# Kernel tuning notes

Hardware: AMD Instinct MI355X
Metric: run time of the kernel (lower is better)

Reference implementation:

```python
import jax, jax.numpy as jnp
import numpy as np

R = 3          # routing iterations (init arg r)
EPS = 1e-7     # init arg epsilon


def squash(s, axis=-1):
    # squash(s) = ||s||^2 / (1 + ||s||^2) * s / (||s|| + EPS)
    n = jnp.linalg.norm(s, axis=axis, keepdims=True)
    n2 = jnp.square(n)
    return (n2 / (1.0 + n2)) * (s / (n + EPS))


def setup_inputs() -> dict:
    key = jax.random.key(0)
    k1, k2 = jax.random.split(key)
    B, S, P, J, I = 32, 32, 2048, 32, 16
    inputs = jax.random.normal(k1, (B, P, I), dtype=jnp.float32)
    # tf.random_normal_initializer default stddev = 0.05
    W = jax.random.normal(k2, (S, P, J, I), dtype=jnp.float32) * 0.05
    return {"inputs": inputs, "W": W}


def reference(inputs, W):
    # u_hat[b,s,p,j] = sum_i W[s,p,j,i] * inputs[b,p,i]
    u_hat = jnp.einsum('spji,bpi->bspj', W, inputs)  # [B,S,P,J]
    B, S, P, J = u_hat.shape
    b = jnp.zeros((B, S, 1, P), dtype=u_hat.dtype)
    v = None
    for _ in range(R):
        c = jax.nn.softmax(b, axis=-1)                     # over primary caps
        s = jnp.einsum('bsxp,bspj->bsxj', c, u_hat)        # [B,S,1,J]
        v = squash(s)                                      # [B,S,1,J]
        agreement = jnp.einsum('bsxj,bspj->bsxp', v, u_hat)  # [B,S,1,P]
        b = b + agreement
    return v.reshape(B, S, J)
```

## Files before the change

kernel.cpp:

```cpp
#include <hip/hip_runtime.h>
#include <stdint.h>

#define B_ 32
#define S_ 32
#define P_ 2048
#define J_ 32
#define I_ 16

typedef _Float16 half8_t __attribute__((ext_vector_type(8)));
typedef float f32x16 __attribute__((ext_vector_type(16)));

__device__ inline float f16lo(uint32_t d) {
    return (float)__builtin_bit_cast(_Float16, (unsigned short)(d & 0xffffu));
}
__device__ inline float f16hi(uint32_t d) {
    return (float)__builtin_bit_cast(_Float16, (unsigned short)(d >> 16));
}

__global__ __launch_bounds__(256) void uhat_kernel(
        const float* __restrict__ W, const float* __restrict__ X,
        uint16_t* __restrict__ U) {
    const int tid  = threadIdx.x;
    const int lane = tid & 63;
    const int wave = tid >> 6;
    const int l31  = lane & 31;
    const int lhi  = lane >> 5;
    const int s    = blockIdx.y;
    const int p0   = blockIdx.x * 16;

    __shared__ uint16_t cs[16384];

    #pragma unroll
    for (int t = 0; t < 4; ++t) {
        const int pl = wave * 4 + t;
        const int p  = p0 + pl;

        const float* wr = W + (((size_t)s * P_ + p) * J_ + l31) * I_ + lhi * 8;
        float4 w0 = *reinterpret_cast<const float4*>(wr);
        float4 w1 = *reinterpret_cast<const float4*>(wr + 4);
        const float* xr = X + ((size_t)l31 * P_ + p) * I_ + lhi * 8;
        float4 x0 = *reinterpret_cast<const float4*>(xr);
        float4 x1 = *reinterpret_cast<const float4*>(xr + 4);

        half8_t A, Bf;
        A[0] = (_Float16)x0.x; A[1] = (_Float16)x0.y;
        A[2] = (_Float16)x0.z; A[3] = (_Float16)x0.w;
        A[4] = (_Float16)x1.x; A[5] = (_Float16)x1.y;
        A[6] = (_Float16)x1.z; A[7] = (_Float16)x1.w;
        Bf[0] = (_Float16)w0.x; Bf[1] = (_Float16)w0.y;
        Bf[2] = (_Float16)w0.z; Bf[3] = (_Float16)w0.w;
        Bf[4] = (_Float16)w1.x; Bf[5] = (_Float16)w1.y;
        Bf[6] = (_Float16)w1.z; Bf[7] = (_Float16)w1.w;

        f32x16 acc = {};
        acc = __builtin_amdgcn_mfma_f32_32x32x16_f16(A, Bf, acc, 0, 0, 0);

        const int swz = ((pl >> 1) & 7) << 4;
        #pragma unroll
        for (int r = 0; r < 16; ++r) {
            const int b = (r & 3) + 8 * (r >> 2) + 4 * lhi;
            const int byteaddr = (b * 1024 + pl * 64 + l31 * 2) ^ swz;
            _Float16 h = (_Float16)acc[r];
            cs[byteaddr >> 1] = __builtin_bit_cast(unsigned short, h);
        }
    }
    __syncthreads();

    const int b   = tid >> 3;
    const int sub = tid & 7;
    uint16_t* gb = U + (((size_t)b * S_ + s) * P_ + p0) * J_;
    #pragma unroll
    for (int k = 0; k < 8; ++k) {
        const int lb = b * 1024 + k * 128 + ((sub ^ k) * 16);
        uint4 v = *reinterpret_cast<const uint4*>(
            reinterpret_cast<const char*>(cs) + lb);
        *reinterpret_cast<uint4*>(
            reinterpret_cast<char*>(gb) + k * 128 + sub * 16) = v;
    }
}

template <int MASK, int HALF>
__device__ inline void red_level(float* red, int lane) {
    const bool hi = (lane & MASK) != 0;
    #pragma unroll
    for (int k = 0; k < HALF; ++k) {
        float send = hi ? red[k] : red[k + HALF];
        float recv = __shfl_xor(send, MASK, 64);
        red[k] = (hi ? red[k + HALF] : red[k]) + recv;
    }
}

__global__ __launch_bounds__(1024) void routing_kernel(
        const uint32_t* __restrict__ U, float* __restrict__ out) {
    const int tid  = threadIdx.x;
    const int lane = tid & 63;
    const int wid  = tid >> 6;
    const int bs   = blockIdx.x;

    __shared__ float sred[16 * 32];
    __shared__ __align__(16) float vlds[32];
    __shared__ float scal[32];

    const uint32_t* ub = U + (size_t)bs * P_ * (J_ / 2) + (size_t)tid * 32;
    uint32_t a[32];
    #pragma unroll
    for (int k = 0; k < 8; ++k) {
        uint4 t = reinterpret_cast<const uint4*>(ub)[k];
        a[k * 4 + 0] = t.x; a[k * 4 + 1] = t.y;
        a[k * 4 + 2] = t.z; a[k * 4 + 3] = t.w;
    }

    float bp0 = 0.0f, bp1 = 0.0f;

    for (int it = 0; it < 3; ++it) {
        float c0, c1;
        if (it == 0) {
            c0 = c1 = 1.0f / 2048.0f;
        } else {
            float m = fmaxf(bp0, bp1);
            #pragma unroll
            for (int msk = 32; msk >= 1; msk >>= 1)
                m = fmaxf(m, __shfl_xor(m, msk, 64));
            if (lane == 0) scal[wid] = m;
            __syncthreads();
            m = scal[0];
            #pragma unroll
            for (int w2 = 1; w2 < 16; ++w2) m = fmaxf(m, scal[w2]);
            float e0 = __expf(bp0 - m);
            float e1 = __expf(bp1 - m);
            float zs = e0 + e1;
            #pragma unroll
            for (int msk = 32; msk >= 1; msk >>= 1)
                zs += __shfl_xor(zs, msk, 64);
            if (lane == 0) scal[16 + wid] = zs;
            __syncthreads();
            float Z = 0.0f;
            #pragma unroll
            for (int w2 = 0; w2 < 16; ++w2) Z += scal[16 + w2];
            float invZ = 1.0f / Z;
            c0 = e0 * invZ;
            c1 = e1 * invZ;
        }

        float red[32];
        #pragma unroll
        for (int k = 0; k < 16; ++k) {
            uint32_t d0 = a[k], d1 = a[16 + k];
            red[2 * k]     = fmaf(c0, f16lo(d0), c1 * f16lo(d1));
            red[2 * k + 1] = fmaf(c0, f16hi(d0), c1 * f16hi(d1));
        }
        red_level<32, 16>(red, lane);
        red_level<16, 8>(red, lane);
        red_level<8, 4>(red, lane);
        red_level<4, 2>(red, lane);
        red_level<2, 1>(red, lane);
        red[0] += __shfl_xor(red[0], 1, 64);
        if ((lane & 1) == 0) sred[wid * 32 + (lane >> 1)] = red[0];
        __syncthreads();

        if (tid < 32) {
            float s = 0.0f;
            #pragma unroll
            for (int w2 = 0; w2 < 16; ++w2) s += sred[w2 * 32 + tid];
            float sq = s * s;
            #pragma unroll
            for (int msk = 16; msk >= 1; msk >>= 1)
                sq += __shfl_xor(sq, msk, 64);
            float n = sqrtf(sq);
            float scale = sq / ((1.0f + sq) * (n + 1e-7f));
            float v = s * scale;
            vlds[tid] = v;
            if (it == 2) out[(size_t)bs * J_ + tid] = v;
        }
        __syncthreads();

        if (it < 2) {
            const float2* vl2 = reinterpret_cast<const float2*>(vlds);
            float ag0 = 0.0f, ag1 = 0.0f;
            #pragma unroll
            for (int k = 0; k < 16; ++k) {
                float2 vk = vl2[k];
                uint32_t d0 = a[k], d1 = a[16 + k];
                ag0 = fmaf(vk.x, f16lo(d0), ag0);
                ag0 = fmaf(vk.y, f16hi(d0), ag0);
                ag1 = fmaf(vk.x, f16lo(d1), ag1);
                ag1 = fmaf(vk.y, f16hi(d1), ag1);
            }
            bp0 += ag0;
            bp1 += ag1;
        }
    }
}

extern "C" void kernel_launch(void* const* d_in, const int* in_sizes, int n_in,
                              void* d_out, int out_size, void* d_ws, size_t ws_size,
                              hipStream_t stream) {
    (void)in_sizes; (void)n_in; (void)out_size;
    const float* X = (const float*)d_in[0];
    const float* W = (const float*)d_in[1];
    float* out     = (float*)d_out;
    uint16_t* U    = (uint16_t*)d_ws;

    const size_t need = (size_t)B_ * S_ * P_ * J_ * 2;
    if (ws_size < need) return;

    dim3 g1(P_ / 16, S_);
    uhat_kernel<<<g1, 256, 0, stream>>>(W, X, U);
    routing_kernel<<<B_ * S_, 1024, 0, stream>>>((const uint32_t*)U, out);
}
```

Measured before the change: 105.1 us.

## Write MFMA output directly in paired-batch plane layout and route two batches per block

```diff
diff --git a/kernel.cpp b/kernel.cpp
--- a/kernel.cpp
+++ b/kernel.cpp
@@ -7,6 +7,8 @@
 #define J_ 32
 #define I_ 16
 
+#define PLSTRIDE ((size_t)S_ * P_ * 32)
+
 typedef _Float16 half8_t __attribute__((ext_vector_type(8)));
 typedef float f32x16 __attribute__((ext_vector_type(16)));
 
@@ -19,63 +21,53 @@
 
 __global__ __launch_bounds__(256) void uhat_kernel(
         const float* __restrict__ W, const float* __restrict__ X,
-        uint16_t* __restrict__ U) {
+        uint32_t* __restrict__ U) {
     const int tid  = threadIdx.x;
     const int lane = tid & 63;
     const int wave = tid >> 6;
     const int l31  = lane & 31;
     const int lhi  = lane >> 5;
     const int s    = blockIdx.y;
-    const int p0   = blockIdx.x * 16;
-
-    __shared__ uint16_t cs[16384];
-
+    const int p0   = blockIdx.x * 16 + wave * 4;
+
+    float4 wv[4][2], xv[4][2];
     #pragma unroll
     for (int t = 0; t < 4; ++t) {
-        const int pl = wave * 4 + t;
-        const int p  = p0 + pl;
-
+        const int p = p0 + t;
         const float* wr = W + (((size_t)s * P_ + p) * J_ + l31) * I_ + lhi * 8;
-        float4 w0 = *reinterpret_cast<const float4*>(wr);
-        float4 w1 = *reinterpret_cast<const float4*>(wr + 4);
+        wv[t][0] = *reinterpret_cast<const float4*>(wr);
+        wv[t][1] = *reinterpret_cast<const float4*>(wr + 4);
         const float* xr = X + ((size_t)l31 * P_ + p) * I_ + lhi * 8;
-        float4 x0 = *reinterpret_cast<const float4*>(xr);
-        float4 x1 = *reinterpret_cast<const float4*>(xr + 4);
-
+        xv[t][0] = *reinterpret_cast<const float4*>(xr);
+        xv[t][1] = *reinterpret_cast<const float4*>(xr + 4);
+    }
+
+    #pragma unroll
+    for (int t = 0; t < 4; ++t) {
+        const int p = p0 + t;
         half8_t A, Bf;
-        A[0] = (_Float16)x0.x; A[1] = (_Float16)x0.y;
-        A[2] = (_Float16)x0.z; A[3] = (_Float16)x0.w;
-        A[4] = (_Float16)x1.x; A[5] = (_Float16)x1.y;
-        A[6] = (_Float16)x1.z; A[7] = (_Float16)x1.w;
-        Bf[0] = (_Float16)w0.x; Bf[1] = (_Float16)w0.y;
-        Bf[2] = (_Float16)w0.z; Bf[3] = (_Float16)w0.w;
-        Bf[4] = (_Float16)w1.x; Bf[5] = (_Float16)w1.y;
-        Bf[6] = (_Float16)w1.z; Bf[7] = (_Float16)w1.w;
+        A[0] = (_Float16)xv[t][0].x; A[1] = (_Float16)xv[t][0].y;
+        A[2] = (_Float16)xv[t][0].z; A[3] = (_Float16)xv[t][0].w;
+        A[4] = (_Float16)xv[t][1].x; A[5] = (_Float16)xv[t][1].y;
+        A[6] = (_Float16)xv[t][1].z; A[7] = (_Float16)xv[t][1].w;
+        Bf[0] = (_Float16)wv[t][0].x; Bf[1] = (_Float16)wv[t][0].y;
+        Bf[2] = (_Float16)wv[t][0].z; Bf[3] = (_Float16)wv[t][0].w;
+        Bf[4] = (_Float16)wv[t][1].x; Bf[5] = (_Float16)wv[t][1].y;
+        Bf[6] = (_Float16)wv[t][1].z; Bf[7] = (_Float16)wv[t][1].w;
 
         f32x16 acc = {};
         acc = __builtin_amdgcn_mfma_f32_32x32x16_f16(A, Bf, acc, 0, 0, 0);
 
-        const int swz = ((pl >> 1) & 7) << 4;
+        const size_t rowbase = ((size_t)s * P_ + p) * 32 + l31;
         #pragma unroll
-        for (int r = 0; r < 16; ++r) {
-            const int b = (r & 3) + 8 * (r >> 2) + 4 * lhi;
-            const int byteaddr = (b * 1024 + pl * 64 + l31 * 2) ^ swz;
-            _Float16 h = (_Float16)acc[r];
-            cs[byteaddr >> 1] = __builtin_bit_cast(unsigned short, h);
-        }
-    }
-    __syncthreads();
-
-    const int b   = tid >> 3;
-    const int sub = tid & 7;
-    uint16_t* gb = U + (((size_t)b * S_ + s) * P_ + p0) * J_;
-    #pragma unroll
-    for (int k = 0; k < 8; ++k) {
-        const int lb = b * 1024 + k * 128 + ((sub ^ k) * 16);
-        uint4 v = *reinterpret_cast<const uint4*>(
-            reinterpret_cast<const char*>(cs) + lb);
-        *reinterpret_cast<uint4*>(
-            reinterpret_cast<char*>(gb) + k * 128 + sub * 16) = v;
+        for (int m = 0; m < 8; ++m) {
+            uint32_t lo = (uint32_t)__builtin_bit_cast(
+                unsigned short, (_Float16)acc[2 * m]);
+            uint32_t hi = (uint32_t)__builtin_bit_cast(
+                unsigned short, (_Float16)acc[2 * m + 1]);
+            const int plane = (m << 1) | lhi;
+            U[(size_t)plane * PLSTRIDE + rowbase] = lo | (hi << 16);
+        }
     }
 }
 
@@ -92,102 +84,124 @@
 
 __global__ __launch_bounds__(1024) void routing_kernel(
         const uint32_t* __restrict__ U, float* __restrict__ out) {
-    const int tid  = threadIdx.x;
-    const int lane = tid & 63;
-    const int wid  = tid >> 6;
-    const int bs   = blockIdx.x;
-
-    __shared__ float sred[16 * 32];
-    __shared__ __align__(16) float vlds[32];
-    __shared__ float scal[32];
-
-    const uint32_t* ub = U + (size_t)bs * P_ * (J_ / 2) + (size_t)tid * 32;
-    uint32_t a[32];
-    #pragma unroll
-    for (int k = 0; k < 8; ++k) {
+    const int tid   = threadIdx.x;
+    const int lane  = tid & 63;
+    const int wid   = tid >> 6;
+    const int plane = blockIdx.x & 15;
+    const int s     = blockIdx.x >> 4;
+    const int m     = plane >> 1;
+    const int lhi   = plane & 1;
+    const int b0    = ((2 * m) & 3) + 8 * (m >> 1) + 4 * lhi;
+
+    __shared__ float sred[2][16][32];
+    __shared__ float vlds[2][32];
+    __shared__ float scal[2][32];
+
+    const uint32_t* ub = U + (size_t)plane * PLSTRIDE
+                           + ((size_t)s * P_ + 2 * (size_t)tid) * 32;
+    uint32_t a[64];
+    #pragma unroll
+    for (int k = 0; k < 16; ++k) {
         uint4 t = reinterpret_cast<const uint4*>(ub)[k];
         a[k * 4 + 0] = t.x; a[k * 4 + 1] = t.y;
         a[k * 4 + 2] = t.z; a[k * 4 + 3] = t.w;
     }
 
-    float bp0 = 0.0f, bp1 = 0.0f;
+    float lg[2][2] = {{0.f, 0.f}, {0.f, 0.f}};
 
     for (int it = 0; it < 3; ++it) {
-        float c0, c1;
+        float c[2][2];
         if (it == 0) {
-            c0 = c1 = 1.0f / 2048.0f;
+            c[0][0] = c[0][1] = c[1][0] = c[1][1] = 1.0f / 2048.0f;
         } else {
-            float m = fmaxf(bp0, bp1);
-            #pragma unroll
-            for (int msk = 32; msk >= 1; msk >>= 1)
-                m = fmaxf(m, __shfl_xor(m, msk, 64));
-            if (lane == 0) scal[wid] = m;
+            #pragma unroll
+            for (int pi = 0; pi < 2; ++pi) {
+                float mx = fmaxf(lg[pi][0], lg[pi][1]);
+                #pragma unroll
+                for (int msk = 32; msk >= 1; msk >>= 1)
+                    mx = fmaxf(mx, __shfl_xor(mx, msk, 64));
+                if (lane == 0) scal[pi][wid] = mx;
+            }
             __syncthreads();
-            m = scal[0];
-            #pragma unroll
-            for (int w2 = 1; w2 < 16; ++w2) m = fmaxf(m, scal[w2]);
-            float e0 = __expf(bp0 - m);
-            float e1 = __expf(bp1 - m);
-            float zs = e0 + e1;
-            #pragma unroll
-            for (int msk = 32; msk >= 1; msk >>= 1)
-                zs += __shfl_xor(zs, msk, 64);
-            if (lane == 0) scal[16 + wid] = zs;
+            float mxf[2];
+            #pragma unroll
+            for (int pi = 0; pi < 2; ++pi) {
+                float mx = scal[pi][0];
+                #pragma unroll
+                for (int w2 = 1; w2 < 16; ++w2) mx = fmaxf(mx, scal[pi][w2]);
+                mxf[pi] = mx;
+                float e0 = __expf(lg[pi][0] - mx);
+                float e1 = __expf(lg[pi][1] - mx);
+                c[pi][0] = e0; c[pi][1] = e1;
+                float zs = e0 + e1;
+                #pragma unroll
+                for (int msk = 32; msk >= 1; msk >>= 1)
+                    zs += __shfl_xor(zs, msk, 64);
+                if (lane == 0) scal[pi][16 + wid] = zs;
+            }
             __syncthreads();
-            float Z = 0.0f;
-            #pragma unroll
-            for (int w2 = 0; w2 < 16; ++w2) Z += scal[16 + w2];
-            float invZ = 1.0f / Z;
-            c0 = e0 * invZ;
-            c1 = e1 * invZ;
-        }
-
-        float red[32];
+            #pragma unroll
+            for (int pi = 0; pi < 2; ++pi) {
+                float Z = 0.0f;
+                #pragma unroll
+                for (int w2 = 0; w2 < 16; ++w2) Z += scal[pi][16 + w2];
+                float invZ = 1.0f / Z;
+                c[pi][0] *= invZ; c[pi][1] *= invZ;
+            }
+        }
+
         #pragma unroll
-        for (int k = 0; k < 16; ++k) {
-            uint32_t d0 = a[k], d1 = a[16 + k];
-            red[2 * k]     = fmaf(c0, f16lo(d0), c1 * f16lo(d1));
-            red[2 * k + 1] = fmaf(c0, f16hi(d0), c1 * f16hi(d1));
-        }
-        red_level<32, 16>(red, lane);
-        red_level<16, 8>(red, lane);
-        red_level<8, 4>(red, lane);
-        red_level<4, 2>(red, lane);
-        red_level<2, 1>(red, lane);
-        red[0] += __shfl_xor(red[0], 1, 64);
-        if ((lane & 1) == 0) sred[wid * 32 + (lane >> 1)] = red[0];
+        for (int pi = 0; pi < 2; ++pi) {
+            float red[32];
+            if (pi == 0) {
+                #pragma unroll
+                for (int j = 0; j < 32; ++j)
+                    red[j] = fmaf(c[0][0], f16lo(a[j]), c[0][1] * f16lo(a[32 + j]));
+            } else {
+                #pragma unroll
+                for (int j = 0; j < 32; ++j)
+                    red[j] = fmaf(c[1][0], f16hi(a[j]), c[1][1] * f16hi(a[32 + j]));
+            }
+            red_level<32, 16>(red, lane);
+            red_level<16, 8>(red, lane);
+            red_level<8, 4>(red, lane);
+            red_level<4, 2>(red, lane);
+            red_level<2, 1>(red, lane);
+            red[0] += __shfl_xor(red[0], 1, 64);
+            if ((lane & 1) == 0) sred[pi][wid][lane >> 1] = red[0];
+        }
         __syncthreads();
 
-        if (tid < 32) {
-            float s = 0.0f;
-            #pragma unroll
-            for (int w2 = 0; w2 < 16; ++w2) s += sred[w2 * 32 + tid];
-            float sq = s * s;
+        if (tid < 64) {
+            const int pi = tid >> 5, j = tid & 31;
+            float sv = 0.0f;
+            #pragma unroll
+            for (int w2 = 0; w2 < 16; ++w2) sv += sred[pi][w2][j];
+            float sq = sv * sv;
             #pragma unroll
             for (int msk = 16; msk >= 1; msk >>= 1)
                 sq += __shfl_xor(sq, msk, 64);
             float n = sqrtf(sq);
             float scale = sq / ((1.0f + sq) * (n + 1e-7f));
-            float v = s * scale;
-            vlds[tid] = v;
-            if (it == 2) out[(size_t)bs * J_ + tid] = v;
+            float v = sv * scale;
+            vlds[pi][j] = v;
+            if (it == 2) out[((size_t)(b0 + pi) * S_ + s) * J_ + j] = v;
         }
         __syncthreads();
 
         if (it < 2) {
-            const float2* vl2 = reinterpret_cast<const float2*>(vlds);
-            float ag0 = 0.0f, ag1 = 0.0f;
-            #pragma unroll
-            for (int k = 0; k < 16; ++k) {
-                float2 vk = vl2[k];
-                uint32_t d0 = a[k], d1 = a[16 + k];
-                ag0 = fmaf(vk.x, f16lo(d0), ag0);
-                ag0 = fmaf(vk.y, f16hi(d0), ag0);
-                ag1 = fmaf(vk.x, f16lo(d1), ag1);
-                ag1 = fmaf(vk.y, f16hi(d1), ag1);
-            }
-            bp0 += ag0;
-            bp1 += ag1;
+            float ag00 = 0.f, ag01 = 0.f, ag10 = 0.f, ag11 = 0.f;
+            #pragma unroll
+            for (int j = 0; j < 32; ++j) {
+                float v0 = vlds[0][j], v1 = vlds[1][j];
+                uint32_t d0 = a[j], d1 = a[32 + j];
+                ag00 = fmaf(v0, f16lo(d0), ag00);
+                ag01 = fmaf(v0, f16lo(d1), ag01);
+                ag10 = fmaf(v1, f16hi(d0), ag10);
+                ag11 = fmaf(v1, f16hi(d1), ag11);
+            }
+            lg[0][0] += ag00; lg[0][1] += ag01;
+            lg[1][0] += ag10; lg[1][1] += ag11;
         }
     }
 }
@@ -199,12 +213,12 @@
     const float* X = (const float*)d_in[0];
     const float* W = (const float*)d_in[1];
     float* out     = (float*)d_out;
-    uint16_t* U    = (uint16_t*)d_ws;
+    uint32_t* U    = (uint32_t*)d_ws;
 
     const size_t need = (size_t)B_ * S_ * P_ * J_ * 2;
     if (ws_size < need) return;
 
     dim3 g1(P_ / 16, S_);
     uhat_kernel<<<g1, 256, 0, stream>>>(W, X, U);
-    routing_kernel<<<B_ * S_, 1024, 0, stream>>>((const uint32_t*)U, out);
-}
+    routing_kernel<<<16 * S_, 1024, 0, stream>>>(U, out);
+}
```

Result: slower. 210.9 us (+100.6%).
